# Optimization experiments

Measured on AMD Instinct MI355X. Metric: run time of the kernel, lower is better.

## Reference

```python
import jax, jax.numpy as jnp
import numpy as np

IN_DIM = 512
HID = IN_DIM // 2
N_SCENES = 64
SEG_LEN = 4096
N = N_SCENES * SEG_LEN
EPS = 1e-5


def setup_inputs() -> dict:
    key = jax.random.key(0)
    ks = jax.random.split(key, 6)
    feats = jax.random.normal(ks[0], (N, IN_DIM), dtype=jnp.float32)
    offsets = (jnp.arange(N_SCENES + 1, dtype=jnp.int32) * SEG_LEN)
    ln_g = jnp.ones((IN_DIM,), jnp.float32) + 0.02 * jax.random.normal(ks[1], (IN_DIM,), jnp.float32)
    ln_b = 0.02 * jax.random.normal(ks[2], (IN_DIM,), jnp.float32)
    w1 = jax.random.normal(ks[3], (HID, IN_DIM), jnp.float32) / np.sqrt(IN_DIM)
    b1 = jnp.zeros((HID,), jnp.float32)
    w2 = jax.random.normal(ks[4], (1, HID), jnp.float32) / np.sqrt(HID)
    b2 = jnp.zeros((1,), jnp.float32)
    return {"feats": feats, "ln_g": ln_g, "ln_b": ln_b, "w1": w1, "b1": b1, "w2": w2, "b2": b2, "offsets": offsets}


def reference(feats, ln_g, ln_b, w1, b1, w2, b2, offsets):
    n = feats.shape[0]
    # segment id per point from prefix-sum offsets
    seg = jnp.searchsorted(offsets, jnp.arange(n, dtype=offsets.dtype), side="right") - 1
    # score MLP: LayerNorm -> Linear -> GELU(exact) -> Linear -> scalar
    mu = jnp.mean(feats, axis=-1, keepdims=True)
    var = jnp.mean(jnp.square(feats - mu), axis=-1, keepdims=True)
    x = (feats - mu) * jax.lax.rsqrt(var + EPS) * ln_g + ln_b
    h = jax.nn.gelu(x @ w1.T + b1, approximate=False)  # [N, HID]
    s = (h @ w2.T + b2)[:, 0]  # [N]
    # segment softmax (stable)
    smax = jax.ops.segment_max(s, seg, num_segments=N_SCENES)
    e = jnp.exp(s - smax[seg])
    denom = jax.ops.segment_sum(e, seg, num_segments=N_SCENES)
    w = e / denom[seg]
    # weighted sum per segment -> [N_SCENES, IN_DIM]
    pooled = jax.ops.segment_sum(feats * w[:, None], seg, num_segments=N_SCENES)
    return pooled
```

## Files before the change

### kernel.cpp

```cpp
#include <hip/hip_runtime.h>

#define IN_DIM 512
#define HID_DIM 256
#define ROWS 32
#define XSS 520
#define PSEG 16
#define PSTRIDE 516

typedef __bf16 bf16x8 __attribute__((ext_vector_type(8)));
typedef unsigned short ushort8 __attribute__((ext_vector_type(8)));
typedef float floatx16 __attribute__((ext_vector_type(16)));

__device__ __forceinline__ unsigned short f2bf_rne(float x) {
    unsigned int u = __float_as_uint(x);
    u += 0x7FFFu + ((u >> 16) & 1u);
    return (unsigned short)(u >> 16);
}
__device__ __forceinline__ unsigned int pack_bf2(float lo, float hi) {
    const unsigned int u0 = __float_as_uint(lo) + 0x8000u;
    const unsigned int u1 = __float_as_uint(hi) + 0x8000u;
    return __builtin_amdgcn_perm(u1, u0, 0x07060302u);
}
__device__ __forceinline__ float gelu(float x) {
    const float ax = fabsf(x) * 0.70710678118654752f;
    const float t = __builtin_amdgcn_rcpf(1.0f + 0.3275911f * ax);
    const float y = t * (0.254829592f +
                    t * (-0.284496736f +
                    t * (1.421413741f +
                    t * (-1.453152027f + t * 1.061405429f))));
    const float e = __expf(-ax * ax);
    float er = 1.0f - y * e;
    er = __builtin_copysignf(er, x);
    return 0.5f * x * (1.0f + er);
}

__global__ void prep_w1_kernel(const float* __restrict__ w1, const float* __restrict__ ln_g,
                               const float* __restrict__ ln_b, const float* __restrict__ b1,
                               unsigned short* __restrict__ w1g, float* __restrict__ gw,
                               float* __restrict__ c1) {
    const int wid = threadIdx.x >> 6;
    const int lane = threadIdx.x & 63;
    const int h = blockIdx.x * 4 + wid;
    const int c8 = lane * 8;
    const float4 wv0 = *(const float4*)(w1 + (size_t)h * IN_DIM + c8);
    const float4 wv1 = *(const float4*)(w1 + (size_t)h * IN_DIM + c8 + 4);
    const float4 g0 = *(const float4*)(ln_g + c8);
    const float4 g1 = *(const float4*)(ln_g + c8 + 4);
    const float4 bb0 = *(const float4*)(ln_b + c8);
    const float4 bb1 = *(const float4*)(ln_b + c8 + 4);
    float wg[8] = {wv0.x * g0.x, wv0.y * g0.y, wv0.z * g0.z, wv0.w * g0.w,
                   wv1.x * g1.x, wv1.y * g1.y, wv1.z * g1.z, wv1.w * g1.w};
    float sg = wg[0] + wg[1] + wg[2] + wg[3] + wg[4] + wg[5] + wg[6] + wg[7];
    float sb = wv0.x * bb0.x + wv0.y * bb0.y + wv0.z * bb0.z + wv0.w * bb0.w +
               wv1.x * bb1.x + wv1.y * bb1.y + wv1.z * bb1.z + wv1.w * bb1.w;
    ushort8 outv;
#pragma unroll
    for (int j = 0; j < 8; j++) outv[j] = f2bf_rne(wg[j]);
    *(ushort8*)(w1g + (size_t)h * IN_DIM + c8) = outv;
    for (int m = 32; m; m >>= 1) {
        sg += __shfl_xor(sg, m);
        sb += __shfl_xor(sb, m);
    }
    if (lane == 0) {
        gw[h] = sg;
        c1[h] = sb + b1[h];
    }
}

__global__ __launch_bounds__(256, 4) void fused_kernel(
    const float* __restrict__ feats, const unsigned short* __restrict__ w1g,
    const float* __restrict__ gw, const float* __restrict__ c1,
    const float* __restrict__ w2, const float* __restrict__ b2,
    const int* __restrict__ offsets, float* __restrict__ partials, int N) {
    __shared__ unsigned short xs[ROWS][XSS];
    __shared__ float spart[4][ROWS];
    __shared__ float2 stats_s[ROWS];
    __shared__ float wbuf[ROWS];
    __shared__ float sMx, sDn, sAl;

    const int tid = threadIdx.x;
    const int wid = tid >> 6;
    const int lane = tid & 63;
    const int l31 = lane & 31;
    const int hi = lane >> 5;
    const int seg = blockIdx.x / PSEG;
    const int part = blockIdx.x % PSEG;
    const int st = offsets[seg];
    const int en = offsets[seg + 1];
    const int len = en - st;
    const int chunk = (len + PSEG - 1) / PSEG;
    const int rs = st + part * chunk;
    const int re = min(rs + chunk, en);
    const int nt = (re > rs) ? ((re - rs + ROWS - 1) / ROWS) : 0;

    const int hid0 = (wid * 2 + 0) * 32 + l31;
    const int hid1 = (wid * 2 + 1) * 32 + l31;
    const float gw0 = gw[hid0], gw1 = gw[hid1];
    const float c10 = c1[hid0], c11 = c1[hid1];
    const float w20 = w2[hid0], w21 = w2[hid1];
    const float b2v = b2[0];

    float O0 = 0.0f, O1 = 0.0f;
    if (tid == 0) { sMx = -3.0e38f; sDn = 0.0f; }

    const int srow4 = tid >> 4;
    const int schunk = tid & 15;

    for (int t = 0; t < nt; t++) {
        const int row0 = rs + t * ROWS;

#pragma unroll
        for (int p = 0; p < 2; p++) {
            const int r = p * 16 + srow4;
            size_t rg = (size_t)(row0 + r);
            if (rg >= (size_t)N) rg = (size_t)N - 1;
            const float* fp = feats + rg * IN_DIM + schunk * 4;
            float4 f[8];
#pragma unroll
            for (int j = 0; j < 8; j++) f[j] = *(const float4*)(fp + j * 64);
            float sf = 0.0f, qf = 0.0f;
#pragma unroll
            for (int j = 0; j < 8; j++) {
                sf += f[j].x + f[j].y + f[j].z + f[j].w;
                qf = fmaf(f[j].x, f[j].x, qf);
                qf = fmaf(f[j].y, f[j].y, qf);
                qf = fmaf(f[j].z, f[j].z, qf);
                qf = fmaf(f[j].w, f[j].w, qf);
            }
#pragma unroll
            for (int j = 0; j < 8; j++) {
                uint2 pk;
                pk.x = pack_bf2(f[j].x, f[j].y);
                pk.y = pack_bf2(f[j].z, f[j].w);
                *(uint2*)&xs[r][j * 64 + schunk * 4] = pk;
            }
#pragma unroll
            for (int m = 1; m < 16; m <<= 1) {
                sf += __shfl_xor(sf, m);
                qf += __shfl_xor(qf, m);
            }
            if (schunk == 0) {
                const float mu = sf * (1.0f / IN_DIM);
                const float var = fmaxf(qf * (1.0f / IN_DIM) - mu * mu, 0.0f);
                stats_s[r] = make_float2(mu, rsqrtf(var + 1e-5f));
            }
        }
        __syncthreads();

        floatx16 acc0 = (floatx16)(0.0f);
        floatx16 acc1 = (floatx16)(0.0f);
        {
            const unsigned short* bp0 = w1g + (size_t)hid0 * IN_DIM + hi * 8;
            const unsigned short* bp1 = w1g + (size_t)hid1 * IN_DIM + hi * 8;
            const unsigned short* ap = &xs[l31][hi * 8];
            bf16x8 b0 = __builtin_bit_cast(bf16x8, *(const ushort8*)bp0);
            bf16x8 b1 = __builtin_bit_cast(bf16x8, *(const ushort8*)bp1);
#pragma unroll 4
            for (int ki = 0; ki < 32; ki++) {
                const bf16x8 a = __builtin_bit_cast(bf16x8, *(const ushort8*)(ap + ki * 16));
                bf16x8 n0 = b0, n1 = b1;
                if (ki < 31) {
                    n0 = __builtin_bit_cast(bf16x8, *(const ushort8*)(bp0 + (ki + 1) * 16));
                    n1 = __builtin_bit_cast(bf16x8, *(const ushort8*)(bp1 + (ki + 1) * 16));
                }
                acc0 = __builtin_amdgcn_mfma_f32_32x32x16_bf16(a, b0, acc0, 0, 0, 0);
                acc1 = __builtin_amdgcn_mfma_f32_32x32x16_bf16(a, b1, acc1, 0, 0, 0);
                b0 = n0;
                b1 = n1;
            }
        }

        float tv[16];
#pragma unroll
        for (int r = 0; r < 16; r++) {
            const int row = (r & 3) + 8 * (r >> 2) + 4 * hi;
            const float2 stt = stats_s[row];
            const float h0 = stt.y * (acc0[r] - stt.x * gw0) + c10;
            const float h1 = stt.y * (acc1[r] - stt.x * gw1) + c11;
            tv[r] = gelu(h0) * w20 + gelu(h1) * w21;
        }
#pragma unroll
        for (int m = 1; m < 32; m <<= 1)
#pragma unroll
            for (int r = 0; r < 16; r++) tv[r] += __shfl_xor(tv[r], m);
        if (l31 == 0) {
#pragma unroll
            for (int r = 0; r < 16; r++)
                spart[wid][(r & 3) + 8 * (r >> 2) + 4 * hi] = tv[r];
        }
        __syncthreads();

        if (tid < 32) {
            float sv = spart[0][tid] + spart[1][tid] + spart[2][tid] + spart[3][tid] + b2v;
            if (row0 + tid >= re) sv = -3.0e38f;
            float mt = sv;
#pragma unroll
            for (int m = 1; m < 32; m <<= 1) mt = fmaxf(mt, __shfl_xor(mt, m));
            const float Mold = sMx;
            const float Mnew = fmaxf(Mold, mt);
            const float al = __expf(Mold - Mnew);
            const float w = __expf(sv - Mnew);
            wbuf[tid] = w;
            float wsum = w;
#pragma unroll
            for (int m = 1; m < 32; m <<= 1) wsum += __shfl_xor(wsum, m);
            if (tid == 0) {
                sDn = sDn * al + wsum;
                sMx = Mnew;
                sAl = al;
            }
        }
        __syncthreads();

        {
            const float al = sAl;
            O0 *= al;
            O1 *= al;
#pragma unroll 8
            for (int r = 0; r < ROWS; r++) {
                const unsigned int d = *(const unsigned int*)&xs[r][tid * 2];
                const float w = wbuf[r];
                O0 = fmaf(w, __uint_as_float(d << 16), O0);
                O1 = fmaf(w, __uint_as_float(d & 0xffff0000u), O1);
            }
        }
        __syncthreads();
    }

    float* pp = partials + (size_t)blockIdx.x * PSTRIDE;
    pp[2 * tid] = O0;
    pp[2 * tid + 1] = O1;
    if (tid == 0) {
        pp[512] = sMx;
        pp[513] = sDn;
    }
}

__global__ void combine_kernel(const float* __restrict__ partials, float* __restrict__ out) {
    const int seg = blockIdx.x;
    const int t = threadIdx.x;
    const float* base = partials + (size_t)seg * PSEG * PSTRIDE;
    float M = -3.0e38f;
#pragma unroll
    for (int p = 0; p < PSEG; p++) M = fmaxf(M, base[p * PSTRIDE + 512]);
    float D = 0.0f, a0 = 0.0f, a1 = 0.0f;
#pragma unroll
    for (int p = 0; p < PSEG; p++) {
        const float e = __expf(base[p * PSTRIDE + 512] - M);
        D += e * base[p * PSTRIDE + 513];
        a0 += e * base[p * PSTRIDE + 2 * t];
        a1 += e * base[p * PSTRIDE + 2 * t + 1];
    }
    out[(size_t)seg * IN_DIM + 2 * t] = a0 / D;
    out[(size_t)seg * IN_DIM + 2 * t + 1] = a1 / D;
}

extern "C" void kernel_launch(void* const* d_in, const int* in_sizes, int n_in,
                              void* d_out, int out_size, void* d_ws, size_t ws_size,
                              hipStream_t stream) {
    const float* feats = (const float*)d_in[0];
    const float* ln_g = (const float*)d_in[1];
    const float* ln_b = (const float*)d_in[2];
    const float* w1 = (const float*)d_in[3];
    const float* b1 = (const float*)d_in[4];
    const float* w2 = (const float*)d_in[5];
    const float* b2 = (const float*)d_in[6];
    const int* offsets = (const int*)d_in[7];
    const int N = in_sizes[0] / IN_DIM;
    const int nseg = in_sizes[7] - 1;
    float* out = (float*)d_out;

    char* ws = (char*)d_ws;
    unsigned short* w1g = (unsigned short*)ws;
    float* gw = (float*)(ws + (size_t)HID_DIM * IN_DIM * 2);
    float* c1 = gw + HID_DIM;
    float* partials = c1 + HID_DIM;

    prep_w1_kernel<<<HID_DIM / 4, 256, 0, stream>>>(w1, ln_g, ln_b, b1, w1g, gw, c1);
    fused_kernel<<<nseg * PSEG, 256, 0, stream>>>(feats, w1g, gw, c1, w2, b2, offsets,
                                                  partials, N);
    combine_kernel<<<nseg, 256, 0, stream>>>(partials, out);
}
```

Before: 882.2 us.

## Use 512-thread blocks with 64-row tiles, register prefetch and per-wave softmax

Doubles the tile to 64 rows and the block to 8 waves, with each wave owning one 32-column slice of the hidden dimension and issuing two MFMAs per shared B fragment. The next tile's features are prefetched into registers while the current tile's GEMM and GELU run. The online softmax is computed redundantly in every wave with register state and shuffles instead of a single-thread shared-memory step. Custom barriers skip the vmem drain, and the number of blocks per segment is halved. This is meant to hide global load latency and remove barriers, at the cost of more registers per thread and fewer blocks in flight.

```diff
diff --git a/kernel.cpp b/kernel.cpp
--- a/kernel.cpp
+++ b/kernel.cpp
@@ -2,9 +2,9 @@
 
 #define IN_DIM 512
 #define HID_DIM 256
-#define ROWS 32
+#define ROWS 64
 #define XSS 520
-#define PSEG 16
+#define PSEG 8
 #define PSTRIDE 516
 
 typedef __bf16 bf16x8 __attribute__((ext_vector_type(8)));
@@ -32,6 +32,13 @@
     float er = 1.0f - y * e;
     er = __builtin_copysignf(er, x);
     return 0.5f * x * (1.0f + er);
+}
+
+__device__ __forceinline__ void barrier_nodrain() {
+    asm volatile("s_waitcnt lgkmcnt(0)" ::: "memory");
+    __builtin_amdgcn_sched_barrier(0);
+    __builtin_amdgcn_s_barrier();
+    __builtin_amdgcn_sched_barrier(0);
 }
 
 __global__ void prep_w1_kernel(const float* __restrict__ w1, const float* __restrict__ ln_g,
@@ -67,16 +74,14 @@
     }
 }
 
-__global__ __launch_bounds__(256, 4) void fused_kernel(
+__global__ __launch_bounds__(512, 4) void fused_kernel(
     const float* __restrict__ feats, const unsigned short* __restrict__ w1g,
     const float* __restrict__ gw, const float* __restrict__ c1,
     const float* __restrict__ w2, const float* __restrict__ b2,
     const int* __restrict__ offsets, float* __restrict__ partials, int N) {
     __shared__ unsigned short xs[ROWS][XSS];
-    __shared__ float spart[4][ROWS];
+    __shared__ float spart[8][ROWS];
     __shared__ float2 stats_s[ROWS];
-    __shared__ float wbuf[ROWS];
-    __shared__ float sMx, sDn, sAl;
 
     const int tid = threadIdx.x;
     const int wid = tid >> 6;
@@ -93,31 +98,40 @@
     const int re = min(rs + chunk, en);
     const int nt = (re > rs) ? ((re - rs + ROWS - 1) / ROWS) : 0;
 
-    const int hid0 = (wid * 2 + 0) * 32 + l31;
-    const int hid1 = (wid * 2 + 1) * 32 + l31;
-    const float gw0 = gw[hid0], gw1 = gw[hid1];
-    const float c10 = c1[hid0], c11 = c1[hid1];
-    const float w20 = w2[hid0], w21 = w2[hid1];
+    const int hid = wid * 32 + l31;
+    const float gw0 = gw[hid];
+    const float c10 = c1[hid];
+    const float w20 = w2[hid];
     const float b2v = b2[0];
 
-    float O0 = 0.0f, O1 = 0.0f;
-    if (tid == 0) { sMx = -3.0e38f; sDn = 0.0f; }
-
-    const int srow4 = tid >> 4;
-    const int schunk = tid & 15;
+    const int srow = tid >> 4;
+    const int sc = tid & 15;
+
+    float O = 0.0f;
+    float Mreg = -3.0e38f, Dreg = 0.0f;
+
+    float4 f[8];
+    if (nt > 0) {
+        int rg = rs + srow;
+        if (rg > N - 1) rg = N - 1;
+        const float* fp = feats + (size_t)rg * IN_DIM + sc * 4;
+#pragma unroll
+        for (int j = 0; j < 8; j++) f[j] = *(const float4*)(fp + j * 64);
+    }
 
     for (int t = 0; t < nt; t++) {
         const int row0 = rs + t * ROWS;
 
-#pragma unroll
-        for (int p = 0; p < 2; p++) {
-            const int r = p * 16 + srow4;
-            size_t rg = (size_t)(row0 + r);
-            if (rg >= (size_t)N) rg = (size_t)N - 1;
-            const float* fp = feats + rg * IN_DIM + schunk * 4;
-            float4 f[8];
-#pragma unroll
-            for (int j = 0; j < 8; j++) f[j] = *(const float4*)(fp + j * 64);
+        float4 g[8];
+        {
+            int rg = row0 + 32 + srow;
+            if (rg > N - 1) rg = N - 1;
+            const float* fp = feats + (size_t)rg * IN_DIM + sc * 4;
+#pragma unroll
+            for (int j = 0; j < 8; j++) g[j] = *(const float4*)(fp + j * 64);
+        }
+
+        {
             float sf = 0.0f, qf = 0.0f;
 #pragma unroll
             for (int j = 0; j < 8; j++) {
@@ -132,17 +146,43 @@
                 uint2 pk;
                 pk.x = pack_bf2(f[j].x, f[j].y);
                 pk.y = pack_bf2(f[j].z, f[j].w);
-                *(uint2*)&xs[r][j * 64 + schunk * 4] = pk;
-            }
-#pragma unroll
-            for (int m = 1; m < 16; m <<= 1) {
-                sf += __shfl_xor(sf, m);
-                qf += __shfl_xor(qf, m);
-            }
-            if (schunk == 0) {
+                *(uint2*)&xs[srow][sc * 4 + j * 64] = pk;
+            }
+            sf += __shfl_xor(sf, 1); qf += __shfl_xor(qf, 1);
+            sf += __shfl_xor(sf, 2); qf += __shfl_xor(qf, 2);
+            sf += __shfl_xor(sf, 4); qf += __shfl_xor(qf, 4);
+            sf += __shfl_xor(sf, 8); qf += __shfl_xor(qf, 8);
+            if (sc == 0) {
                 const float mu = sf * (1.0f / IN_DIM);
                 const float var = fmaxf(qf * (1.0f / IN_DIM) - mu * mu, 0.0f);
-                stats_s[r] = make_float2(mu, rsqrtf(var + 1e-5f));
+                stats_s[srow] = make_float2(mu, rsqrtf(var + 1e-5f));
+            }
+        }
+        {
+            float sf = 0.0f, qf = 0.0f;
+#pragma unroll
+            for (int j = 0; j < 8; j++) {
+                sf += g[j].x + g[j].y + g[j].z + g[j].w;
+                qf = fmaf(g[j].x, g[j].x, qf);
+                qf = fmaf(g[j].y, g[j].y, qf);
+                qf = fmaf(g[j].z, g[j].z, qf);
+                qf = fmaf(g[j].w, g[j].w, qf);
+            }
+#pragma unroll
+            for (int j = 0; j < 8; j++) {
+                uint2 pk;
+                pk.x = pack_bf2(g[j].x, g[j].y);
+                pk.y = pack_bf2(g[j].z, g[j].w);
+                *(uint2*)&xs[32 + srow][sc * 4 + j * 64] = pk;
+            }
+            sf += __shfl_xor(sf, 1); qf += __shfl_xor(qf, 1);
+            sf += __shfl_xor(sf, 2); qf += __shfl_xor(qf, 2);
+            sf += __shfl_xor(sf, 4); qf += __shfl_xor(qf, 4);
+            sf += __shfl_xor(sf, 8); qf += __shfl_xor(qf, 8);
+            if (sc == 0) {
+                const float mu = sf * (1.0f / IN_DIM);
+                const float var = fmaxf(qf * (1.0f / IN_DIM) - mu * mu, 0.0f);
+                stats_s[32 + srow] = make_float2(mu, rsqrtf(var + 1e-5f));
             }
         }
         __syncthreads();
@@ -150,89 +190,106 @@
         floatx16 acc0 = (floatx16)(0.0f);
         floatx16 acc1 = (floatx16)(0.0f);
         {
-            const unsigned short* bp0 = w1g + (size_t)hid0 * IN_DIM + hi * 8;
-            const unsigned short* bp1 = w1g + (size_t)hid1 * IN_DIM + hi * 8;
-            const unsigned short* ap = &xs[l31][hi * 8];
-            bf16x8 b0 = __builtin_bit_cast(bf16x8, *(const ushort8*)bp0);
-            bf16x8 b1 = __builtin_bit_cast(bf16x8, *(const ushort8*)bp1);
-#pragma unroll 4
-            for (int ki = 0; ki < 32; ki++) {
-                const bf16x8 a = __builtin_bit_cast(bf16x8, *(const ushort8*)(ap + ki * 16));
-                bf16x8 n0 = b0, n1 = b1;
-                if (ki < 31) {
-                    n0 = __builtin_bit_cast(bf16x8, *(const ushort8*)(bp0 + (ki + 1) * 16));
-                    n1 = __builtin_bit_cast(bf16x8, *(const ushort8*)(bp1 + (ki + 1) * 16));
+            const unsigned short* bp = w1g + (size_t)hid * IN_DIM + hi * 8;
+            const unsigned short* ap0 = &xs[l31][hi * 8];
+            const unsigned short* ap1 = &xs[32 + l31][hi * 8];
+            ushort8 br[8];
+#pragma unroll
+            for (int i = 0; i < 8; i++) br[i] = *(const ushort8*)(bp + i * 16);
+#pragma unroll
+            for (int kg = 0; kg < 4; kg++) {
+#pragma unroll
+                for (int u = 0; u < 8; u++) {
+                    const int ki = kg * 8 + u;
+                    const bf16x8 a0 = __builtin_bit_cast(bf16x8, *(const ushort8*)(ap0 + ki * 16));
+                    const bf16x8 a1 = __builtin_bit_cast(bf16x8, *(const ushort8*)(ap1 + ki * 16));
+                    const bf16x8 bv = __builtin_bit_cast(bf16x8, br[u]);
+                    acc0 = __builtin_amdgcn_mfma_f32_32x32x16_bf16(a0, bv, acc0, 0, 0, 0);
+                    acc1 = __builtin_amdgcn_mfma_f32_32x32x16_bf16(a1, bv, acc1, 0, 0, 0);
+                    if (ki + 8 < 32)
+                        br[u] = *(const ushort8*)(bp + (ki + 8) * 16);
                 }
-                acc0 = __builtin_amdgcn_mfma_f32_32x32x16_bf16(a, b0, acc0, 0, 0, 0);
-                acc1 = __builtin_amdgcn_mfma_f32_32x32x16_bf16(a, b1, acc1, 0, 0, 0);
-                b0 = n0;
-                b1 = n1;
-            }
-        }
-
-        float tv[16];
-#pragma unroll
-        for (int r = 0; r < 16; r++) {
-            const int row = (r & 3) + 8 * (r >> 2) + 4 * hi;
-            const float2 stt = stats_s[row];
-            const float h0 = stt.y * (acc0[r] - stt.x * gw0) + c10;
-            const float h1 = stt.y * (acc1[r] - stt.x * gw1) + c11;
-            tv[r] = gelu(h0) * w20 + gelu(h1) * w21;
-        }
-#pragma unroll
-        for (int m = 1; m < 32; m <<= 1)
-#pragma unroll
-            for (int r = 0; r < 16; r++) tv[r] += __shfl_xor(tv[r], m);
-        if (l31 == 0) {
-#pragma unroll
-            for (int r = 0; r < 16; r++)
-                spart[wid][(r & 3) + 8 * (r >> 2) + 4 * hi] = tv[r];
-        }
-        __syncthreads();
-
-        if (tid < 32) {
-            float sv = spart[0][tid] + spart[1][tid] + spart[2][tid] + spart[3][tid] + b2v;
-            if (row0 + tid >= re) sv = -3.0e38f;
+            }
+        }
+
+        {
+            float tv[16];
+#pragma unroll
+            for (int q = 0; q < 16; q++) {
+                const int rowl = (q & 3) + 8 * (q >> 2) + 4 * hi;
+                const float2 stt = stats_s[rowl];
+                const float h = stt.y * (acc0[q] - stt.x * gw0) + c10;
+                tv[q] = gelu(h) * w20;
+            }
+#pragma unroll
+            for (int m = 1; m < 32; m <<= 1)
+#pragma unroll
+                for (int q = 0; q < 16; q++) tv[q] += __shfl_xor(tv[q], m);
+            if (l31 == 0) {
+#pragma unroll
+                for (int q = 0; q < 16; q++)
+                    spart[wid][(q & 3) + 8 * (q >> 2) + 4 * hi] = tv[q];
+            }
+#pragma unroll
+            for (int q = 0; q < 16; q++) {
+                const int rowl = 32 + (q & 3) + 8 * (q >> 2) + 4 * hi;
+                const float2 stt = stats_s[rowl];
+                const float h = stt.y * (acc1[q] - stt.x * gw0) + c10;
+                tv[q] = gelu(h) * w20;
+            }
+#pragma unroll
+            for (int m = 1; m < 32; m <<= 1)
+#pragma unroll
+                for (int q = 0; q < 16; q++) tv[q] += __shfl_xor(tv[q], m);
+            if (l31 == 0) {
+#pragma unroll
+                for (int q = 0; q < 16; q++)
+                    spart[wid][32 + (q & 3) + 8 * (q >> 2) + 4 * hi] = tv[q];
+            }
+        }
+
+        if (t + 1 < nt) {
+            int rg = row0 + ROWS + srow;
+            if (rg > N - 1) rg = N - 1;
+            const float* fp = feats + (size_t)rg * IN_DIM + sc * 4;
+#pragma unroll
+            for (int j = 0; j < 8; j++) f[j] = *(const float4*)(fp + j * 64);
+        }
+        barrier_nodrain();
+
+        float wv_, al;
+        {
+            float sv = spart[0][lane] + spart[1][lane] + spart[2][lane] + spart[3][lane] +
+                       spart[4][lane] + spart[5][lane] + spart[6][lane] + spart[7][lane] + b2v;
+            if (row0 + lane >= re) sv = -3.0e38f;
             float mt = sv;
 #pragma unroll
-            for (int m = 1; m < 32; m <<= 1) mt = fmaxf(mt, __shfl_xor(mt, m));
-            const float Mold = sMx;
-            const float Mnew = fmaxf(Mold, mt);
-            const float al = __expf(Mold - Mnew);
-            const float w = __expf(sv - Mnew);
-            wbuf[tid] = w;
-            float wsum = w;
-#pragma unroll
-            for (int m = 1; m < 32; m <<= 1) wsum += __shfl_xor(wsum, m);
-            if (tid == 0) {
-                sDn = sDn * al + wsum;
-                sMx = Mnew;
-                sAl = al;
-            }
-        }
-        __syncthreads();
-
-        {
-            const float al = sAl;
-            O0 *= al;
-            O1 *= al;
-#pragma unroll 8
-            for (int r = 0; r < ROWS; r++) {
-                const unsigned int d = *(const unsigned int*)&xs[r][tid * 2];
-                const float w = wbuf[r];
-                O0 = fmaf(w, __uint_as_float(d << 16), O0);
-                O1 = fmaf(w, __uint_as_float(d & 0xffff0000u), O1);
-            }
-        }
-        __syncthreads();
+            for (int m = 1; m < 64; m <<= 1) mt = fmaxf(mt, __shfl_xor(mt, m));
+            const float Mnew = fmaxf(Mreg, mt);
+            al = __expf(Mreg - Mnew);
+            wv_ = __expf(sv - Mnew);
+            float ws = wv_;
+#pragma unroll
+            for (int m = 1; m < 64; m <<= 1) ws += __shfl_xor(ws, m);
+            Dreg = Dreg * al + ws;
+            Mreg = Mnew;
+        }
+
+        O *= al;
+#pragma unroll 16
+        for (int rr = 0; rr < ROWS; rr++) {
+            const float wr = __shfl(wv_, rr);
+            const unsigned int us = (unsigned int)xs[rr][tid];
+            O = fmaf(wr, __uint_as_float(us << 16), O);
+        }
+        if (t + 1 < nt) barrier_nodrain();
     }
 
     float* pp = partials + (size_t)blockIdx.x * PSTRIDE;
-    pp[2 * tid] = O0;
-    pp[2 * tid + 1] = O1;
+    pp[tid] = O;
     if (tid == 0) {
-        pp[512] = sMx;
-        pp[513] = sDn;
+        pp[512] = Mreg;
+        pp[513] = Dreg;
     }
 }
 
@@ -277,7 +334,7 @@
     float* partials = c1 + HID_DIM;
 
     prep_w1_kernel<<<HID_DIM / 4, 256, 0, stream>>>(w1, ln_g, ln_b, b1, w1g, gw, c1);
-    fused_kernel<<<nseg * PSEG, 256, 0, stream>>>(feats, w1g, gw, c1, w2, b2, offsets,
+    fused_kernel<<<nseg * PSEG, 512, 0, stream>>>(feats, w1g, gw, c1, w2, b2, offsets,
                                                   partials, N);
     combine_kernel<<<nseg, 256, 0, stream>>>(partials, out);
 }
```

After: 1.061 ms. 20.2% more time.
